# Optimization experiments

Measured on AMD Instinct MI355X. Metric: run time of the kernel, lower is better.

The kernel has to match this reference:

```python
import jax, jax.numpy as jnp
import numpy as np

B, S, T = 256, 1024, 128

def setup_inputs() -> dict:
    key = jax.random.key(0)
    k1, k2, k3, k4, k5 = jax.random.split(key, 5)
    return {
        "emissions": jax.random.normal(k1, (B, S, T), dtype=jnp.float32),
        "tags": jax.random.randint(k2, (B, S), 0, T, dtype=jnp.int64 if jax.config.jax_enable_x64 else jnp.int32),
        "mask": jnp.ones((B, S), dtype=jnp.float32),
        "start_transitions": jax.random.normal(k3, (T,), dtype=jnp.float32),
        "end_transitions": jax.random.normal(k4, (T,), dtype=jnp.float32),
        "transitions": jax.random.normal(k5, (T, T), dtype=jnp.float32),
    }


def _gold_score(emissions, tags, mask, start_transitions, end_transitions, transitions):
    # score of the gold tag sequence (note: original uses log_softmax'd emissions here)
    score = start_transitions[tags[:, 0]]
    logp = jax.nn.log_softmax(emissions, axis=2)
    em_sc = jnp.take_along_axis(logp, tags[:, :, None], axis=2)[:, :, 0] * mask  # [B,S]
    score = score + em_sc.sum(axis=1)
    trans_sc = transitions[tags[:, :-1], tags[:, 1:]] * mask[:, 1:]  # [B,S-1]
    score = score + trans_sc.sum(axis=1)
    score = score + end_transitions[tags[:, -1]] * mask[:, -1]
    return score


def _forward_score(emissions, mask, start_transitions, end_transitions, transitions):
    # partition function via forward algorithm (faithful to original, incl. its
    # masking quirk: alpha recurrence is unmasked; only the last step's masked
    # alpha is used for the final logsumexp)
    alpha0 = start_transitions + emissions[:, 0]  # [B,T]

    def step(carry, inp):
        alpha, _ = carry
        em_t, m_t = inp  # [B,T], [B]
        # [B,T_prev,T_cur] broadcast add, logsumexp over prev tag
        new_alpha = jax.nn.logsumexp(
            alpha[:, :, None] + transitions[None, :, :] + em_t[:, None, :], axis=1
        )
        return (new_alpha, new_alpha * m_t[:, None]), None

    xs = (jnp.swapaxes(emissions[:, 1:], 0, 1), jnp.swapaxes(mask[:, 1:], 0, 1))
    (_, alpha_masked), _ = jax.lax.scan(step, (alpha0, jnp.zeros_like(alpha0)), xs)
    return jax.nn.logsumexp(alpha_masked + end_transitions, axis=1)  # [B]


def reference(emissions, tags, mask, start_transitions, end_transitions, transitions):
    score = _gold_score(emissions, tags, mask, start_transitions, end_transitions, transitions)
    fwd = _forward_score(emissions, mask, start_transitions, end_transitions, transitions)
    return jnp.mean(fwd - score)
```

## Files before the change

kernel.cpp:

```cpp
#include <hip/hip_runtime.h>

#define CRF_B 256
#define CRF_S 1024
#define CRF_T 128

typedef __attribute__((ext_vector_type(4))) float f32x4;

__device__ __forceinline__ void barrier_lds_only() {
    __asm__ volatile("s_waitcnt lgkmcnt(0)\n\ts_barrier" ::: "memory");
}

__device__ __forceinline__ float dpp_add_xor1(float x) {
    int y = __builtin_amdgcn_mov_dpp(__float_as_int(x), 0xB1, 0xF, 0xF, false);
    return x + __int_as_float(y);
}
__device__ __forceinline__ float dpp_add_xor2(float x) {
    int y = __builtin_amdgcn_mov_dpp(__float_as_int(x), 0x4E, 0xF, 0xF, false);
    return x + __int_as_float(y);
}
__device__ __forceinline__ float dpp_add_xor4u(float x) {
    int y = __builtin_amdgcn_mov_dpp(__float_as_int(x), 0x141, 0xF, 0xF, false);
    return x + __int_as_float(y);
}

__device__ __forceinline__ f32x4 exp4(f32x4 v) {
    f32x4 r;
    r.x = __expf(v.x); r.y = __expf(v.y); r.z = __expf(v.z); r.w = __expf(v.w);
    return r;
}
__device__ __forceinline__ float hsum4(f32x4 v) {
    return (v.x + v.y) + (v.z + v.w);
}

__global__ __launch_bounds__(256) void crf_gold_kernel(
    const float* __restrict__ em, const int* __restrict__ tags,
    const float* __restrict__ mask, const float* __restrict__ startT,
    const float* __restrict__ endT, const float* __restrict__ trans,
    float* __restrict__ out)
{
    const int b = blockIdx.x;
    const int tid = threadIdx.x;
    const int p = tid & 3;
    const int q = tid >> 2;
    const int* tg = tags + (size_t)b * CRF_S;
    const float* mk = mask + (size_t)b * CRF_S;
    const float* emr = em + (size_t)b * CRF_S * CRF_T;

    float g_acc = 0.f;
#pragma unroll
    for (int k = 0; k < 4; ++k) {
        int t = tid + k * 256;
        int tagt = tg[t];
        float m = mk[t];
        g_acc += emr[(size_t)t * CRF_T + tagt] * m;
        if (t >= 1) g_acc += trans[tg[t - 1] * CRF_T + tagt] * m;
    }
    if (tid == 0) {
        g_acc += startT[tg[0]];
        g_acc += endT[tg[CRF_S - 1]] * mk[CRF_S - 1];
    }

    float s2 = 0.f;
#pragma unroll 1
    for (int it = 0; it < 16; ++it) {
        const int r = it * 64 + q;
        const float* row = emr + (size_t)r * CRF_T;
        f32x4 sum4 = {0.f, 0.f, 0.f, 0.f};
#pragma unroll
        for (int k = 0; k < 8; ++k)
            sum4 += exp4(*(const f32x4*)(row + k * 16 + p * 4));
        float s = hsum4(sum4);
        s = dpp_add_xor1(s);
        s = dpp_add_xor2(s);
        if (p == 0) s2 += __logf(s) * mk[r];
    }

    float contrib = s2 - g_acc;
#pragma unroll
    for (int d = 1; d < 64; d <<= 1) contrib += __shfl_xor(contrib, d);
    __shared__ float r4[4];
    if ((tid & 63) == 0) r4[tid >> 6] = contrib;
    __syncthreads();
    if (tid == 0) {
        float tot = (r4[0] + r4[1]) + (r4[2] + r4[3]);
        atomicAdd(out, tot * (1.0f / CRF_B));
    }
}

__global__ __launch_bounds__(256, 1) void crf_fwd_kernel(
    const float* __restrict__ em, const float* __restrict__ mask,
    const float* __restrict__ startT, const float* __restrict__ endT,
    const float* __restrict__ trans, float* __restrict__ out)
{
    const int b = blockIdx.x;
    const int tid = threadIdx.x;
    const int r = tid & 7;
    const int cq = tid >> 3;
    const int j0 = cq * 4;
    const bool leader = (r == 0);

    __shared__ __align__(16) float Abuf[2][CRF_T];
    __shared__ __align__(16) float partsA[32];
    __shared__ float red[8];
    __shared__ float lzsh;

    int kidx[4];
#pragma unroll
    for (int k = 0; k < 4; ++k) kidx[k] = (k + r) & 3;

    f32x4 EE[4][4];
#pragma unroll
    for (int k = 0; k < 4; ++k) {
#pragma unroll
        for (int s = 0; s < 4; ++s) {
            const int i = r * 16 + kidx[k] * 4 + s;
            f32x4 t4 = *(const f32x4*)&trans[i * CRF_T + j0];
            EE[k][0][s] = __expf(t4.x);
            EE[k][1][s] = __expf(t4.y);
            EE[k][2][s] = __expf(t4.z);
            EE[k][3][s] = __expf(t4.w);
        }
    }

    const float* emb = em + (size_t)b * CRF_S * CRF_T + j0;
    const float mlast = mask[(size_t)b * CRF_S + (CRF_S - 1)];

    float logZ = 0.f;
    float rc = 1.f;

    f32x4 emv[4], eh[2][4];
#pragma unroll
    for (int k = 0; k < 4; ++k) emv[k] = *(const f32x4*)(emb + (size_t)k * CRF_T);
#pragma unroll
    for (int k = 0; k < 4; ++k) eh[0][k] = exp4(emv[k]);
#pragma unroll
    for (int k = 0; k < 4; ++k) emv[k] = *(const f32x4*)(emb + (size_t)(4 + k) * CRF_T);

    auto STEP = [&](int t, int role, f32x4 ehv) {
        const int rb = (t & 1) ^ 1, wb = t & 1;

        if (role == 3 && leader && t < 1023) {
            const f32x4* pa = (const f32x4*)partsA;
            f32x4 s8 = ((pa[0] + pa[1]) + (pa[2] + pa[3])) +
                       ((pa[4] + pa[5]) + (pa[6] + pa[7]));
            float c = hsum4(s8);
            rc = __builtin_amdgcn_rcpf(c);
            logZ += __logf(c);
        }

        const f32x4* Ab = (const f32x4*)&Abuf[rb][r * 16];
        f32x4 ac0 = {0.f, 0.f, 0.f, 0.f}, ac1 = ac0, ac2 = ac0, ac3 = ac0;
#pragma unroll
        for (int k = 0; k < 4; ++k) {
            f32x4 av = Ab[kidx[k]];
            ac0 = __builtin_elementwise_fma(av, EE[k][0], ac0);
            ac1 = __builtin_elementwise_fma(av, EE[k][1], ac1);
            ac2 = __builtin_elementwise_fma(av, EE[k][2], ac2);
            ac3 = __builtin_elementwise_fma(av, EE[k][3], ac3);
        }
        float d0 = hsum4(ac0), d1 = hsum4(ac1), d2 = hsum4(ac2), d3 = hsum4(ac3);
        d0 = dpp_add_xor4u(dpp_add_xor2(dpp_add_xor1(d0)));
        d1 = dpp_add_xor4u(dpp_add_xor2(dpp_add_xor1(d1)));
        d2 = dpp_add_xor4u(dpp_add_xor2(dpp_add_xor1(d2)));
        d3 = dpp_add_xor4u(dpp_add_xor2(dpp_add_xor1(d3)));

        float a0 = d0 * ehv.x, a1 = d1 * ehv.y, a2 = d2 * ehv.z, a3 = d3 * ehv.w;
        if (role == 0) { a0 *= rc; a1 *= rc; a2 *= rc; a3 *= rc; }
        if (leader) {
            f32x4 av = {a0, a1, a2, a3};
            *(f32x4*)&Abuf[wb][j0] = av;
            if (role == 2) partsA[cq] = (a0 + a1) + (a2 + a3);
        }
        barrier_lds_only();
    };

    {
        f32x4 s4 = *(const f32x4*)&startT[j0];
        if (leader) {
            f32x4 a;
            a.x = __expf(s4.x) * eh[0][0].x;
            a.y = __expf(s4.y) * eh[0][0].y;
            a.z = __expf(s4.z) * eh[0][0].z;
            a.w = __expf(s4.w) * eh[0][0].w;
            *(f32x4*)&Abuf[0][j0] = a;
        }
        barrier_lds_only();
        STEP(1, 1, eh[0][1]);
#pragma unroll
        for (int k = 0; k < 4; ++k) eh[1][k] = exp4(emv[k]);
        STEP(2, 2, eh[0][2]);
#pragma unroll
        for (int k = 0; k < 4; ++k) emv[k] = *(const f32x4*)(emb + (size_t)(8 + k) * CRF_T);
        STEP(3, 3, eh[0][3]);
    }

#pragma unroll 1
    for (int g = 1; g < 256; ++g) {
        const int t0 = 4 * g;
        const int cur = g & 1, nxt = cur ^ 1;
        STEP(t0 + 0, 0, eh[cur][0]);
        STEP(t0 + 1, 1, eh[cur][1]);
        if (g <= 254) {
#pragma unroll
            for (int k = 0; k < 4; ++k) eh[nxt][k] = exp4(emv[k]);
        }
        STEP(t0 + 2, 2, eh[cur][2]);
        if (g <= 253) {
#pragma unroll
            for (int k = 0; k < 4; ++k)
                emv[k] = *(const f32x4*)(emb + (size_t)(t0 + 8 + k) * CRF_T);
        }
        STEP(t0 + 3, 3, eh[cur][3]);
    }

    __syncthreads();
    if (tid == 0) lzsh = logZ;
    __syncthreads();
    const float lz = lzsh;

    float v = -3.0e38f;
    if (tid < 128)
        v = (__logf(Abuf[1][tid]) + lz) * mlast + endT[tid];
    float mx = v;
#pragma unroll
    for (int dd = 1; dd < 64; dd <<= 1) mx = fmaxf(mx, __shfl_xor(mx, dd));
    if ((tid & 63) == 0) red[tid >> 6] = mx;
    __syncthreads();
    mx = fmaxf(fmaxf(red[0], red[1]), fmaxf(red[2], red[3]));
    float ex = (tid < 128) ? __expf(v - mx) : 0.f;
#pragma unroll
    for (int dd = 1; dd < 64; dd <<= 1) ex += __shfl_xor(ex, dd);
    if ((tid & 63) == 0) red[4 + (tid >> 6)] = ex;
    __syncthreads();
    if (tid == 0) {
        float sm = (red[4] + red[5]) + (red[6] + red[7]);
        float fwd = mx + __logf(sm);
        atomicAdd(out, fwd * (1.0f / CRF_B));
    }
}

extern "C" void kernel_launch(void* const* d_in, const int* in_sizes, int n_in,
                              void* d_out, int out_size, void* d_ws, size_t ws_size,
                              hipStream_t stream)
{
    const float* em     = (const float*)d_in[0];
    const int*   tags   = (const int*)d_in[1];
    const float* mask   = (const float*)d_in[2];
    const float* startT = (const float*)d_in[3];
    const float* endT   = (const float*)d_in[4];
    const float* trans  = (const float*)d_in[5];
    float* out = (float*)d_out;

    hipMemsetAsync(out, 0, sizeof(float), stream);
    hipLaunchKernelGGL(crf_gold_kernel, dim3(CRF_B), dim3(256), 0, stream,
                       em, tags, mask, startT, endT, trans, out);
    hipLaunchKernelGGL(crf_fwd_kernel, dim3(CRF_B), dim3(256), 0, stream,
                       em, mask, startT, endT, trans, out);
}
```

Baseline: 596.5 us.

## Split gold-score kernel across sequence slices and pack two CRF chains per block

The gold-score kernel now launches eight blocks per batch element, each covering 128 timesteps, instead of one block per sequence. The goal is more parallelism for the bandwidth-bound log-softmax and gather pass. The forward-recurrence kernel now runs two batch chains per 512-thread block, with per-chain LDS buffers. This halves the block count so each CU interleaves two latency-bound recurrences. The cost is that the shared barrier now couples eight waves from two independent chains, and half the CUs may sit idle.

```diff
diff --git a/kernel.cpp b/kernel.cpp
--- a/kernel.cpp
+++ b/kernel.cpp
@@ -3,6 +3,8 @@
 #define CRF_B 256
 #define CRF_S 1024
 #define CRF_T 128
+#define CH 2
+#define GSPLIT 8
 
 typedef __attribute__((ext_vector_type(4))) float f32x4;
 
@@ -38,7 +40,9 @@
     const float* __restrict__ endT, const float* __restrict__ trans,
     float* __restrict__ out)
 {
-    const int b = blockIdx.x;
+    const int b     = blockIdx.x >> 3;
+    const int slice = blockIdx.x & (GSPLIT - 1);
+    const int base  = slice << 7;
     const int tid = threadIdx.x;
     const int p = tid & 3;
     const int q = tid >> 2;
@@ -47,23 +51,22 @@
     const float* emr = em + (size_t)b * CRF_S * CRF_T;
 
     float g_acc = 0.f;
-#pragma unroll
-    for (int k = 0; k < 4; ++k) {
-        int t = tid + k * 256;
-        int tagt = tg[t];
-        float m = mk[t];
+    if (tid < 128) {
+        const int t = base + tid;
+        const int tagt = tg[t];
+        const float m = mk[t];
         g_acc += emr[(size_t)t * CRF_T + tagt] * m;
         if (t >= 1) g_acc += trans[tg[t - 1] * CRF_T + tagt] * m;
     }
-    if (tid == 0) {
+    if (tid == 0 && slice == 0)
         g_acc += startT[tg[0]];
+    if (tid == 0 && slice == GSPLIT - 1)
         g_acc += endT[tg[CRF_S - 1]] * mk[CRF_S - 1];
-    }
 
     float s2 = 0.f;
-#pragma unroll 1
-    for (int it = 0; it < 16; ++it) {
-        const int r = it * 64 + q;
+#pragma unroll
+    for (int it = 0; it < 2; ++it) {
+        const int r = base + it * 64 + q;
         const float* row = emr + (size_t)r * CRF_T;
         f32x4 sum4 = {0.f, 0.f, 0.f, 0.f};
 #pragma unroll
@@ -87,22 +90,24 @@
     }
 }
 
-__global__ __launch_bounds__(256, 1) void crf_fwd_kernel(
+__global__ __launch_bounds__(256 * CH, 1) void crf_fwd_kernel(
     const float* __restrict__ em, const float* __restrict__ mask,
     const float* __restrict__ startT, const float* __restrict__ endT,
     const float* __restrict__ trans, float* __restrict__ out)
 {
-    const int b = blockIdx.x;
     const int tid = threadIdx.x;
-    const int r = tid & 7;
-    const int cq = tid >> 3;
+    const int chain = tid >> 8;
+    const int ct = tid & 255;
+    const int b = blockIdx.x * CH + chain;
+    const int r = ct & 7;
+    const int cq = ct >> 3;
     const int j0 = cq * 4;
     const bool leader = (r == 0);
 
-    __shared__ __align__(16) float Abuf[2][CRF_T];
-    __shared__ __align__(16) float partsA[32];
-    __shared__ float red[8];
-    __shared__ float lzsh;
+    __shared__ __align__(16) float Abuf[CH][2][CRF_T];
+    __shared__ __align__(16) float partsA[CH][32];
+    __shared__ float red[CH][8];
+    __shared__ float lzsh[CH];
 
     int kidx[4];
 #pragma unroll
@@ -140,7 +145,7 @@
         const int rb = (t & 1) ^ 1, wb = t & 1;
 
         if (role == 3 && leader && t < 1023) {
-            const f32x4* pa = (const f32x4*)partsA;
+            const f32x4* pa = (const f32x4*)partsA[chain];
             f32x4 s8 = ((pa[0] + pa[1]) + (pa[2] + pa[3])) +
                        ((pa[4] + pa[5]) + (pa[6] + pa[7]));
             float c = hsum4(s8);
@@ -148,7 +153,7 @@
             logZ += __logf(c);
         }
 
-        const f32x4* Ab = (const f32x4*)&Abuf[rb][r * 16];
+        const f32x4* Ab = (const f32x4*)&Abuf[chain][rb][r * 16];
         f32x4 ac0 = {0.f, 0.f, 0.f, 0.f}, ac1 = ac0, ac2 = ac0, ac3 = ac0;
 #pragma unroll
         for (int k = 0; k < 4; ++k) {
@@ -168,8 +173,8 @@
         if (role == 0) { a0 *= rc; a1 *= rc; a2 *= rc; a3 *= rc; }
         if (leader) {
             f32x4 av = {a0, a1, a2, a3};
-            *(f32x4*)&Abuf[wb][j0] = av;
-            if (role == 2) partsA[cq] = (a0 + a1) + (a2 + a3);
+            *(f32x4*)&Abuf[chain][wb][j0] = av;
+            if (role == 2) partsA[chain][cq] = (a0 + a1) + (a2 + a3);
         }
         barrier_lds_only();
     };
@@ -182,7 +187,7 @@
             a.y = __expf(s4.y) * eh[0][0].y;
             a.z = __expf(s4.z) * eh[0][0].z;
             a.w = __expf(s4.w) * eh[0][0].w;
-            *(f32x4*)&Abuf[0][j0] = a;
+            *(f32x4*)&Abuf[chain][0][j0] = a;
         }
         barrier_lds_only();
         STEP(1, 1, eh[0][1]);
@@ -214,26 +219,27 @@
     }
 
     __syncthreads();
-    if (tid == 0) lzsh = logZ;
-    __syncthreads();
-    const float lz = lzsh;
+    if (ct == 0) lzsh[chain] = logZ;
+    __syncthreads();
+    const float lz = lzsh[chain];
 
     float v = -3.0e38f;
-    if (tid < 128)
-        v = (__logf(Abuf[1][tid]) + lz) * mlast + endT[tid];
+    if (ct < 128)
+        v = (__logf(Abuf[chain][1][ct]) + lz) * mlast + endT[ct];
     float mx = v;
 #pragma unroll
     for (int dd = 1; dd < 64; dd <<= 1) mx = fmaxf(mx, __shfl_xor(mx, dd));
-    if ((tid & 63) == 0) red[tid >> 6] = mx;
-    __syncthreads();
-    mx = fmaxf(fmaxf(red[0], red[1]), fmaxf(red[2], red[3]));
-    float ex = (tid < 128) ? __expf(v - mx) : 0.f;
+    if ((ct & 63) == 0) red[chain][ct >> 6] = mx;
+    __syncthreads();
+    mx = fmaxf(fmaxf(red[chain][0], red[chain][1]),
+               fmaxf(red[chain][2], red[chain][3]));
+    float ex = (ct < 128) ? __expf(v - mx) : 0.f;
 #pragma unroll
     for (int dd = 1; dd < 64; dd <<= 1) ex += __shfl_xor(ex, dd);
-    if ((tid & 63) == 0) red[4 + (tid >> 6)] = ex;
-    __syncthreads();
-    if (tid == 0) {
-        float sm = (red[4] + red[5]) + (red[6] + red[7]);
+    if ((ct & 63) == 0) red[chain][4 + (ct >> 6)] = ex;
+    __syncthreads();
+    if (ct == 0) {
+        float sm = (red[chain][4] + red[chain][5]) + (red[chain][6] + red[chain][7]);
         float fwd = mx + __logf(sm);
         atomicAdd(out, fwd * (1.0f / CRF_B));
     }
@@ -252,8 +258,8 @@
     float* out = (float*)d_out;
 
     hipMemsetAsync(out, 0, sizeof(float), stream);
-    hipLaunchKernelGGL(crf_gold_kernel, dim3(CRF_B), dim3(256), 0, stream,
+    hipLaunchKernelGGL(crf_gold_kernel, dim3(CRF_B * GSPLIT), dim3(256), 0, stream,
                        em, tags, mask, startT, endT, trans, out);
-    hipLaunchKernelGGL(crf_fwd_kernel, dim3(CRF_B), dim3(256), 0, stream,
+    hipLaunchKernelGGL(crf_fwd_kernel, dim3(CRF_B / CH), dim3(256 * CH), 0, stream,
                        em, mask, startT, endT, trans, out);
 }
```

New measurement: 757.5 us. +27.0%, slower.

## Fuse gold and forward kernels into one launch with split gold blocks

Applied to the files above, without the earlier changes.

Merges the gold-score and forward-recursion kernels into one grid: 256 forward blocks run first, followed by gold work split eight ways per sequence so it fills the idle CUs alongside the serial forward blocks. The forward block shrinks to 128 threads with 4 lanes per output group, each lane doing 8 FMA chunks, so the cross-lane DPP reduction loses a stage and the barrier covers fewer waves. Per-block partials are written to a workspace and summed by a small reduction kernel, which replaces the memset and atomics. The cost is more registers for the exp(transitions) tile, an extra kernel launch, and a need for enough workspace.

```diff
diff --git a/kernel.cpp b/kernel.cpp
--- a/kernel.cpp
+++ b/kernel.cpp
@@ -3,6 +3,11 @@
 #define CRF_B 256
 #define CRF_S 1024
 #define CRF_T 128
+#define GSPLIT 8
+#define NFWD   CRF_B
+#define NGOLD  (CRF_B * GSPLIT)
+#define WS_FWD (CRF_B * GSPLIT)
+#define WS_N   (WS_FWD + CRF_B)
 
 typedef __attribute__((ext_vector_type(4))) float f32x4;
 
@@ -16,10 +21,6 @@
 }
 __device__ __forceinline__ float dpp_add_xor2(float x) {
     int y = __builtin_amdgcn_mov_dpp(__float_as_int(x), 0x4E, 0xF, 0xF, false);
-    return x + __int_as_float(y);
-}
-__device__ __forceinline__ float dpp_add_xor4u(float x) {
-    int y = __builtin_amdgcn_mov_dpp(__float_as_int(x), 0x141, 0xF, 0xF, false);
     return x + __int_as_float(y);
 }
 
@@ -32,88 +33,32 @@
     return (v.x + v.y) + (v.z + v.w);
 }
 
-__global__ __launch_bounds__(256) void crf_gold_kernel(
-    const float* __restrict__ em, const int* __restrict__ tags,
-    const float* __restrict__ mask, const float* __restrict__ startT,
-    const float* __restrict__ endT, const float* __restrict__ trans,
-    float* __restrict__ out)
-{
-    const int b = blockIdx.x;
-    const int tid = threadIdx.x;
-    const int p = tid & 3;
-    const int q = tid >> 2;
-    const int* tg = tags + (size_t)b * CRF_S;
-    const float* mk = mask + (size_t)b * CRF_S;
-    const float* emr = em + (size_t)b * CRF_S * CRF_T;
-
-    float g_acc = 0.f;
-#pragma unroll
-    for (int k = 0; k < 4; ++k) {
-        int t = tid + k * 256;
-        int tagt = tg[t];
-        float m = mk[t];
-        g_acc += emr[(size_t)t * CRF_T + tagt] * m;
-        if (t >= 1) g_acc += trans[tg[t - 1] * CRF_T + tagt] * m;
-    }
-    if (tid == 0) {
-        g_acc += startT[tg[0]];
-        g_acc += endT[tg[CRF_S - 1]] * mk[CRF_S - 1];
-    }
-
-    float s2 = 0.f;
-#pragma unroll 1
-    for (int it = 0; it < 16; ++it) {
-        const int r = it * 64 + q;
-        const float* row = emr + (size_t)r * CRF_T;
-        f32x4 sum4 = {0.f, 0.f, 0.f, 0.f};
-#pragma unroll
-        for (int k = 0; k < 8; ++k)
-            sum4 += exp4(*(const f32x4*)(row + k * 16 + p * 4));
-        float s = hsum4(sum4);
-        s = dpp_add_xor1(s);
-        s = dpp_add_xor2(s);
-        if (p == 0) s2 += __logf(s) * mk[r];
-    }
-
-    float contrib = s2 - g_acc;
-#pragma unroll
-    for (int d = 1; d < 64; d <<= 1) contrib += __shfl_xor(contrib, d);
-    __shared__ float r4[4];
-    if ((tid & 63) == 0) r4[tid >> 6] = contrib;
-    __syncthreads();
-    if (tid == 0) {
-        float tot = (r4[0] + r4[1]) + (r4[2] + r4[3]);
-        atomicAdd(out, tot * (1.0f / CRF_B));
-    }
-}
-
-__global__ __launch_bounds__(256, 1) void crf_fwd_kernel(
+__device__ __forceinline__ void fwd_block(
+    const int b, const int tid,
     const float* __restrict__ em, const float* __restrict__ mask,
     const float* __restrict__ startT, const float* __restrict__ endT,
-    const float* __restrict__ trans, float* __restrict__ out)
-{
-    const int b = blockIdx.x;
-    const int tid = threadIdx.x;
-    const int r = tid & 7;
-    const int cq = tid >> 3;
+    const float* __restrict__ trans, float* __restrict__ ws)
+{
+    const int r  = tid & 3;
+    const int cq = tid >> 2;
     const int j0 = cq * 4;
     const bool leader = (r == 0);
 
     __shared__ __align__(16) float Abuf[2][CRF_T];
     __shared__ __align__(16) float partsA[32];
-    __shared__ float red[8];
+    __shared__ float red[4];
     __shared__ float lzsh;
 
-    int kidx[4];
-#pragma unroll
-    for (int k = 0; k < 4; ++k) kidx[k] = (k + r) & 3;
-
-    f32x4 EE[4][4];
-#pragma unroll
-    for (int k = 0; k < 4; ++k) {
+    int kidx[8];
+#pragma unroll
+    for (int k = 0; k < 8; ++k) kidx[k] = (k + 2 * r) & 7;
+
+    f32x4 EE[8][4];
+#pragma unroll
+    for (int k = 0; k < 8; ++k) {
 #pragma unroll
         for (int s = 0; s < 4; ++s) {
-            const int i = r * 16 + kidx[k] * 4 + s;
+            const int i = 32 * r + 4 * kidx[k] + s;
             f32x4 t4 = *(const f32x4*)&trans[i * CRF_T + j0];
             EE[k][0][s] = __expf(t4.x);
             EE[k][1][s] = __expf(t4.y);
@@ -148,27 +93,31 @@
             logZ += __logf(c);
         }
 
-        const f32x4* Ab = (const f32x4*)&Abuf[rb][r * 16];
-        f32x4 ac0 = {0.f, 0.f, 0.f, 0.f}, ac1 = ac0, ac2 = ac0, ac3 = ac0;
-#pragma unroll
-        for (int k = 0; k < 4; ++k) {
-            f32x4 av = Ab[kidx[k]];
+        const f32x4* A4 = (const f32x4*)&Abuf[rb][32 * r];
+        f32x4 av = A4[kidx[0]];
+        f32x4 ac0 = av * EE[0][0];
+        f32x4 ac1 = av * EE[0][1];
+        f32x4 ac2 = av * EE[0][2];
+        f32x4 ac3 = av * EE[0][3];
+#pragma unroll
+        for (int k = 1; k < 8; ++k) {
+            av = A4[kidx[k]];
             ac0 = __builtin_elementwise_fma(av, EE[k][0], ac0);
             ac1 = __builtin_elementwise_fma(av, EE[k][1], ac1);
             ac2 = __builtin_elementwise_fma(av, EE[k][2], ac2);
             ac3 = __builtin_elementwise_fma(av, EE[k][3], ac3);
         }
         float d0 = hsum4(ac0), d1 = hsum4(ac1), d2 = hsum4(ac2), d3 = hsum4(ac3);
-        d0 = dpp_add_xor4u(dpp_add_xor2(dpp_add_xor1(d0)));
-        d1 = dpp_add_xor4u(dpp_add_xor2(dpp_add_xor1(d1)));
-        d2 = dpp_add_xor4u(dpp_add_xor2(dpp_add_xor1(d2)));
-        d3 = dpp_add_xor4u(dpp_add_xor2(dpp_add_xor1(d3)));
+        d0 = dpp_add_xor2(dpp_add_xor1(d0));
+        d1 = dpp_add_xor2(dpp_add_xor1(d1));
+        d2 = dpp_add_xor2(dpp_add_xor1(d2));
+        d3 = dpp_add_xor2(dpp_add_xor1(d3));
 
         float a0 = d0 * ehv.x, a1 = d1 * ehv.y, a2 = d2 * ehv.z, a3 = d3 * ehv.w;
         if (role == 0) { a0 *= rc; a1 *= rc; a2 *= rc; a3 *= rc; }
         if (leader) {
-            f32x4 av = {a0, a1, a2, a3};
-            *(f32x4*)&Abuf[wb][j0] = av;
+            f32x4 avw = {a0, a1, a2, a3};
+            *(f32x4*)&Abuf[wb][j0] = avw;
             if (role == 2) partsA[cq] = (a0 + a1) + (a2 + a3);
         }
         barrier_lds_only();
@@ -218,25 +167,104 @@
     __syncthreads();
     const float lz = lzsh;
 
-    float v = -3.0e38f;
-    if (tid < 128)
-        v = (__logf(Abuf[1][tid]) + lz) * mlast + endT[tid];
+    float v = (__logf(Abuf[1][tid]) + lz) * mlast + endT[tid];
     float mx = v;
 #pragma unroll
     for (int dd = 1; dd < 64; dd <<= 1) mx = fmaxf(mx, __shfl_xor(mx, dd));
     if ((tid & 63) == 0) red[tid >> 6] = mx;
     __syncthreads();
-    mx = fmaxf(fmaxf(red[0], red[1]), fmaxf(red[2], red[3]));
-    float ex = (tid < 128) ? __expf(v - mx) : 0.f;
+    mx = fmaxf(red[0], red[1]);
+    float ex = __expf(v - mx);
 #pragma unroll
     for (int dd = 1; dd < 64; dd <<= 1) ex += __shfl_xor(ex, dd);
-    if ((tid & 63) == 0) red[4 + (tid >> 6)] = ex;
-    __syncthreads();
-    if (tid == 0) {
-        float sm = (red[4] + red[5]) + (red[6] + red[7]);
-        float fwd = mx + __logf(sm);
-        atomicAdd(out, fwd * (1.0f / CRF_B));
-    }
+    if ((tid & 63) == 0) red[2 + (tid >> 6)] = ex;
+    __syncthreads();
+    if (tid == 0)
+        ws[WS_FWD + b] = mx + __logf(red[2] + red[3]);
+}
+
+__device__ __forceinline__ void gold_block(
+    const int gb, const int tid,
+    const float* __restrict__ em, const int* __restrict__ tags,
+    const float* __restrict__ mask, const float* __restrict__ startT,
+    const float* __restrict__ endT, const float* __restrict__ trans,
+    float* __restrict__ ws)
+{
+    const int b     = gb >> 3;
+    const int slice = gb & (GSPLIT - 1);
+    const int base  = slice << 7;
+    const int p = tid & 3;
+    const int q = tid >> 2;
+    const int* tg = tags + (size_t)b * CRF_S;
+    const float* mk = mask + (size_t)b * CRF_S;
+    const float* emr = em + (size_t)b * CRF_S * CRF_T;
+
+    __shared__ float r2g[2];
+
+    float g_acc = 0.f;
+    {
+        const int t = base + tid;
+        const int tagt = tg[t];
+        const float m = mk[t];
+        g_acc += emr[(size_t)t * CRF_T + tagt] * m;
+        if (t >= 1) g_acc += trans[tg[t - 1] * CRF_T + tagt] * m;
+    }
+    if (tid == 0 && slice == 0)
+        g_acc += startT[tg[0]];
+    if (tid == 0 && slice == GSPLIT - 1)
+        g_acc += endT[tg[CRF_S - 1]] * mk[CRF_S - 1];
+
+    float s2 = 0.f;
+#pragma unroll
+    for (int it = 0; it < 4; ++it) {
+        const int rr = base + it * 32 + q;
+        const float* row = emr + (size_t)rr * CRF_T;
+        f32x4 sum4 = {0.f, 0.f, 0.f, 0.f};
+#pragma unroll
+        for (int k = 0; k < 8; ++k)
+            sum4 += exp4(*(const f32x4*)(row + k * 16 + p * 4));
+        float s = hsum4(sum4);
+        s = dpp_add_xor1(s);
+        s = dpp_add_xor2(s);
+        if (p == 0) s2 += __logf(s) * mk[rr];
+    }
+
+    float contrib = s2 - g_acc;
+#pragma unroll
+    for (int d = 1; d < 64; d <<= 1) contrib += __shfl_xor(contrib, d);
+    if ((tid & 63) == 0) r2g[tid >> 6] = contrib;
+    __syncthreads();
+    if (tid == 0)
+        ws[gb] = r2g[0] + r2g[1];
+}
+
+__global__ __launch_bounds__(128, 1) void crf_main_kernel(
+    const float* __restrict__ em, const int* __restrict__ tags,
+    const float* __restrict__ mask, const float* __restrict__ startT,
+    const float* __restrict__ endT, const float* __restrict__ trans,
+    float* __restrict__ ws)
+{
+    if (blockIdx.x < NFWD)
+        fwd_block(blockIdx.x, threadIdx.x, em, mask, startT, endT, trans, ws);
+    else
+        gold_block(blockIdx.x - NFWD, threadIdx.x, em, tags, mask, startT,
+                   endT, trans, ws);
+}
+
+__global__ __launch_bounds__(256) void crf_reduce_kernel(
+    const float* __restrict__ ws, float* __restrict__ out)
+{
+    const int tid = threadIdx.x;
+    float s = 0.f;
+#pragma unroll
+    for (int k = 0; k < WS_N; k += 256) s += ws[k + tid];
+#pragma unroll
+    for (int d = 1; d < 64; d <<= 1) s += __shfl_xor(s, d);
+    __shared__ float r4[4];
+    if ((tid & 63) == 0) r4[tid >> 6] = s;
+    __syncthreads();
+    if (tid == 0)
+        out[0] = ((r4[0] + r4[1]) + (r4[2] + r4[3])) * (1.0f / CRF_B);
 }
 
 extern "C" void kernel_launch(void* const* d_in, const int* in_sizes, int n_in,
@@ -250,10 +278,10 @@
     const float* endT   = (const float*)d_in[4];
     const float* trans  = (const float*)d_in[5];
     float* out = (float*)d_out;
-
-    hipMemsetAsync(out, 0, sizeof(float), stream);
-    hipLaunchKernelGGL(crf_gold_kernel, dim3(CRF_B), dim3(256), 0, stream,
-                       em, tags, mask, startT, endT, trans, out);
-    hipLaunchKernelGGL(crf_fwd_kernel, dim3(CRF_B), dim3(256), 0, stream,
-                       em, mask, startT, endT, trans, out);
-}
+    float* ws  = (float*)d_ws;
+
+    hipLaunchKernelGGL(crf_main_kernel, dim3(NFWD + NGOLD), dim3(128), 0, stream,
+                       em, tags, mask, startT, endT, trans, ws);
+    hipLaunchKernelGGL(crf_reduce_kernel, dim3(1), dim3(256), 0, stream,
+                       ws, out);
+}
```

After: 597.1 us. No clear change (+0.1%).
